# Kernel optimization log

Hardware: AMD Instinct MI355X
Metric: run time of the kernel (lower is better)

## Reference

```python
import jax, jax.numpy as jnp
import numpy as np

B, S, E, H = 2, 2048, 1024, 16
D = E // H  # head_dim = 64


def setup_inputs() -> dict:
    key = jax.random.key(0)
    ks = jax.random.split(key, 6)
    scale = 1.0 / np.sqrt(E)
    return {
        "x": jax.random.normal(ks[0], (B, S, E), dtype=jnp.float32),
        "Wqkv_w": jax.random.normal(ks[1], (3 * E, E), dtype=jnp.float32) * scale,
        "Wqkv_b": jax.random.normal(ks[2], (3 * E,), dtype=jnp.float32) * 0.01,
        "out_w": jax.random.normal(ks[3], (E, E), dtype=jnp.float32) * scale,
        "out_b": jax.random.normal(ks[4], (E,), dtype=jnp.float32) * 0.01,
        "distance_decay": jax.random.normal(ks[5], (1,), dtype=jnp.float32),
    }


def reference(x, Wqkv_w, Wqkv_b, out_w, out_b, distance_decay):
    b, s, e = x.shape
    # fused QKV projection: (b, s, 3e) -> three (b, h, s, d)
    qkv = x @ Wqkv_w.T + Wqkv_b
    qkv = qkv.reshape(b, s, 3, H, D).transpose(2, 0, 3, 1, 4)  # (3, b, h, s, d)
    q, k, v = qkv[0], qkv[1], qkv[2]
    # scores scaled by 1/sqrt(head_dim)
    scores = jnp.einsum("bhsd,bhtd->bhst", q, k) / jnp.sqrt(jnp.asarray(D, x.dtype))
    # multiplicative exponential distance decay: exp(-|a| * |i-j|)
    idx = jnp.arange(s, dtype=x.dtype)
    dist = jnp.abs(idx[:, None] - idx[None, :])  # (s, s)
    decay = jnp.exp(-jnp.abs(distance_decay[0]) * dist)
    scores = scores * decay  # broadcast over (b, h)
    attn = jax.nn.softmax(scores, axis=-1)
    out = jnp.einsum("bhst,bhtd->bhsd", attn, v)  # (b, h, s, d)
    out = out.transpose(0, 2, 1, 3).reshape(b, s, e)  # (b, s, e)
    return out @ out_w.T + out_b
```

## Files before the change

### kernel.cpp

```cpp
#include <hip/hip_runtime.h>
#include <hip/hip_bf16.h>

#define BN 2
#define SDIM 2048
#define EDIM 1024
#define HN 16
#define DDIM 64

typedef __attribute__((ext_vector_type(8))) short bfrag;
typedef __attribute__((ext_vector_type(4))) float ffrag;

__device__ __forceinline__ ffrag mfma16(bfrag a, bfrag b, ffrag c) {
    return __builtin_amdgcn_mfma_f32_16x16x32_bf16(a, b, c, 0, 0, 0);
}

__device__ __forceinline__ ushort f2bf(float f) {
    union { float f; unsigned u; } un;
    un.f = f;
    unsigned u = un.u;
    u += 0x7fffu + ((u >> 16) & 1u);
    return (ushort)(u >> 16);
}

__device__ __forceinline__ uint pkbf2(float a, float b) {
    __hip_bfloat162 h = __float22bfloat162_rn(make_float2(a, b));
    union { __hip_bfloat162 h; uint u; } cv;
    cv.h = h;
    return cv.u;
}

__device__ __forceinline__ void gld16(const void* g, void* l) {
    __builtin_amdgcn_global_load_lds((const __attribute__((address_space(1))) void*)g,
                                     (__attribute__((address_space(3))) void*)l,
                                     16, 0, 0);
}

__global__ __launch_bounds__(256) void to_bf16_3(const float* __restrict__ a, ushort* __restrict__ oa, int na,
                                                 const float* __restrict__ b, ushort* __restrict__ ob, int nb,
                                                 const float* __restrict__ c, ushort* __restrict__ oc, int nc) {
    int i = (blockIdx.x * 256 + threadIdx.x) * 4;
    const float* src;
    ushort* dst;
    if (i < na)                { src = a + i;            dst = oa + i; }
    else if (i < na + nb)      { src = b + (i - na);     dst = ob + (i - na); }
    else if (i < na + nb + nc) { src = c + (i - na - nb); dst = oc + (i - na - nb); }
    else return;
    float4 v = *(const float4*)src;
    uint2 u;
    u.x = pkbf2(v.x, v.y);
    u.y = pkbf2(v.z, v.w);
    *(uint2*)dst = u;
}

template <int MODE, int MI>
__global__ __launch_bounds__(256) void gemm_bt(const ushort* __restrict__ A,
                                               const ushort* __restrict__ Bt,
                                               const float* __restrict__ bias,
                                               void* __restrict__ Cout,
                                               int M, int N, int K) {
    __shared__ ushort As[MI * 32 * 32];
    __shared__ ushort Bs[128 * 32];

    const int tid  = threadIdx.x;
    const int wave = tid >> 6;
    const int lane = tid & 63;
    const int ln16 = lane & 15;
    const int quad = lane >> 4;
    const int wm = wave >> 1, wn = wave & 1;
    const int bm = blockIdx.x * (MI * 32);
    const int bn = blockIdx.y * 128;

    ffrag acc[MI][4];
#pragma unroll
    for (int mi = 0; mi < MI; ++mi)
#pragma unroll
        for (int ni = 0; ni < 4; ++ni)
            acc[mi][ni] = (ffrag){0.f, 0.f, 0.f, 0.f};

    for (int k0 = 0; k0 < K; k0 += 32) {
#pragma unroll
        for (int p = 0; p < MI / 2; ++p) {
            int g0 = p * 256 + wave * 64;
            int g  = g0 + lane;
            int r  = g >> 2;
            int c  = ((g & 3) - (r >> 1)) & 3;
            gld16(A + (size_t)(bm + r) * K + k0 + c * 8, (ushort*)As + g0 * 8);
        }
#pragma unroll
        for (int p = 0; p < 2; ++p) {
            int g0 = p * 256 + wave * 64;
            int g  = g0 + lane;
            int r  = g >> 2;
            int c  = ((g & 3) - (r >> 1)) & 3;
            gld16(Bt + (size_t)(bn + r) * K + k0 + c * 8, (ushort*)Bs + g0 * 8);
        }
        __syncthreads();

        bfrag af[MI], bf[4];
#pragma unroll
        for (int mi = 0; mi < MI; ++mi) {
            int r = wm * (MI * 16) + mi * 16 + ln16;
            af[mi] = *(const bfrag*)&As[r * 32 + ((quad + (r >> 1)) & 3) * 8];
        }
#pragma unroll
        for (int ni = 0; ni < 4; ++ni) {
            int r = wn * 64 + ni * 16 + ln16;
            bf[ni] = *(const bfrag*)&Bs[r * 32 + ((quad + (r >> 1)) & 3) * 8];
        }
#pragma unroll
        for (int mi = 0; mi < MI; ++mi)
#pragma unroll
            for (int ni = 0; ni < 4; ++ni)
                acc[mi][ni] = mfma16(af[mi], bf[ni], acc[mi][ni]);
        __syncthreads();
    }

#pragma unroll
    for (int mi = 0; mi < MI; ++mi) {
#pragma unroll
        for (int ni = 0; ni < 4; ++ni) {
            int col = bn + wn * 64 + ni * 16 + ln16;
            float bc = bias[col];
            int row0 = bm + wm * (MI * 16) + mi * 16 + quad * 4;
            if (MODE == 0) {
#pragma unroll
                for (int reg = 0; reg < 4; ++reg)
                    ((float*)Cout)[(size_t)(row0 + reg) * N + col] = acc[mi][ni][reg] + bc;
            } else {
                int which = col >> 10;
                int rem = col & 1023;
                int h = rem >> 6;
                int d = rem & 63;
                int b = row0 >> 11;
                int s0 = row0 & 2047;
                if (which == 2) {
                    float v0 = acc[mi][ni][0] + bc, v1 = acc[mi][ni][1] + bc;
                    float v2 = acc[mi][ni][2] + bc, v3 = acc[mi][ni][3] + bc;
                    uint2 pk;
                    pk.x = pkbf2(v0, v1);
                    pk.y = pkbf2(v2, v3);
                    size_t dst = 2ull * (BN * HN * SDIM * DDIM) +
                                 (((size_t)(b * HN + h)) * DDIM + d) * SDIM + s0;
                    *(uint2*)((ushort*)Cout + dst) = pk;
                } else {
                    float sc = (which == 0) ? 0.125f : 1.f;
#pragma unroll
                    for (int reg = 0; reg < 4; ++reg) {
                        float v = (acc[mi][ni][reg] + bc) * sc;
                        size_t dst = (size_t)which * (BN * HN * SDIM * DDIM) +
                                     (((size_t)(b * HN + h)) * SDIM + s0 + reg) * DDIM + d;
                        ((ushort*)Cout)[dst] = f2bf(v);
                    }
                }
            }
        }
    }
}

__global__ __launch_bounds__(64) void vsum_prefix(const ushort* __restrict__ Vtb,
                                                  float* __restrict__ PS) {
    const int bh = blockIdx.x;
    const int d  = threadIdx.x;
    const ushort* row = Vtb + ((size_t)bh * DDIM + d) * SDIM;
    float* ps = PS + (size_t)bh * 33 * 64;
    float run = 0.f;
    for (int k = 0; k < 32; ++k) {
        ps[k * 64 + d] = run;
        float s = 0.f;
#pragma unroll
        for (int j = 0; j < 64; j += 8) {
            uint4 v = *(const uint4*)(row + k * 64 + j);
            ushort tmp[8];
            *(uint4*)tmp = v;
#pragma unroll
            for (int e = 0; e < 8; ++e) {
                union { float f; uint u; } c;
                c.u = ((uint)tmp[e]) << 16;
                s += c.f;
            }
        }
        run += s;
    }
    ps[32 * 64 + d] = run;
}

__global__ __launch_bounds__(512, 4) void flash_attn(const ushort* __restrict__ Qb,
                                                     const ushort* __restrict__ Kb,
                                                     const ushort* __restrict__ Vtb,
                                                     const float* __restrict__ decay_ptr,
                                                     const float* __restrict__ PS,
                                                     ushort* __restrict__ Ob) {
    __shared__ ushort KVs[2][2][4096];
    __shared__ ushort Pb[128][72];
    __shared__ float  Fv[64];

    const int tid  = threadIdx.x;
    const int wave = tid >> 6;
    const int lane = tid & 63;
    const int ln16 = lane & 15;
    const int quad = lane >> 4;

    const int bh = blockIdx.y;
    const int q0 = blockIdx.x * 128;
    const size_t head_off = (size_t)bh * SDIM * DDIM;
    const float absa = fabsf(decay_ptr[0]);
    const float LOG2E = 1.442695041f;
    const float M0L2 = -17.3123404f;
    const float E12 = 6.144212353e-6f;

    int Dstar = (absa > 1e-5f) ? (int)ceilf(16.0f / absa) : (4 * SDIM);
    int lo = q0 - 63 - Dstar; if (lo < 0) lo = 0;
    int hi = q0 + 127 + Dstar; if (hi > SDIM - 1) hi = SDIM - 1;
    const int tlo = lo >> 6;
    const int thi = hi >> 6;
    const int ntiles = thi - tlo + 1;

    if (tid < 64) {
        const float* ps = PS + (size_t)bh * 33 * 64;
        Fv[tid] = ps[tlo * 64 + tid] + ps[32 * 64 + tid] - ps[(thi + 1) * 64 + tid];
    }

    auto stageKV = [&](int t0, int buf) {
        int g0 = wave * 64;
        int g  = g0 + lane;
        int r  = g >> 3;
        int c  = (g - r) & 7;
        gld16(Kb  + head_off + (size_t)(t0 + r) * DDIM + c * 8,
              (ushort*)&KVs[buf][0][0] + g0 * 8);
        gld16(Vtb + head_off + (size_t)r * SDIM + t0 + c * 8,
              (ushort*)&KVs[buf][1][0] + g0 * 8);
    };

#pragma unroll
    for (int p = 0; p < 2; ++p) {
        int idx = p * 512 + tid;
        int r = idx >> 3, c = (idx & 7) * 8;
        *(uint4*)&Pb[r][c] = *(const uint4*)(Qb + head_off + (size_t)(q0 + r) * DDIM + c);
    }
    stageKV(tlo * 64, 0);
    __syncthreads();

    bfrag aq[2];
#pragma unroll
    for (int kb = 0; kb < 2; ++kb)
        aq[kb] = *(const bfrag*)&Pb[wave * 16 + ln16][kb * 32 + quad * 8];

    bfrag ones;
#pragma unroll
    for (int i = 0; i < 8; ++i) ones[i] = (short)0x3F80;

    float EcB[4], FcB[4], Epw[4], Fpw[4];
#pragma unroll
    for (int reg = 0; reg < 4; ++reg) {
        int cr = quad * 4 + reg;
        EcB[reg] = __expf(-absa * (float)(15 - cr));
        FcB[reg] = __expf(-absa * (float)cr);
    }
#pragma unroll
    for (int ni = 0; ni < 4; ++ni) {
        Epw[ni] = __expf(-absa * (float)(16 * (3 - ni)));
        Fpw[ni] = __expf(-absa * (float)(16 * ni));
    }
    const float Er = __expf(-absa * (float)ln16);
    const float Fr = __expf(-absa * (float)(15 - ln16));

    ffrag lacc = (ffrag){0.f, 0.f, 0.f, 0.f};
    ffrag o[4];
#pragma unroll
    for (int ni = 0; ni < 4; ++ni) o[ni] = (ffrag){0.f, 0.f, 0.f, 0.f};

    const int m = wave * 16 + ln16;

    for (int it = 0; it < ntiles; ++it) {
        const int t0 = (tlo + it) * 64;
        const int buf = it & 1;
        if (it + 1 < ntiles) stageKV(t0 + 64, buf ^ 1);

        const ushort* Kt = &KVs[buf][0][0];
        const ushort* Vt = &KVs[buf][1][0];

        ffrag sc[4];
#pragma unroll
        for (int ni = 0; ni < 4; ++ni) {
            ffrag a = (ffrag){0.f, 0.f, 0.f, 0.f};
            const int rk = ni * 16 + ln16;
#pragma unroll
            for (int kb = 0; kb < 2; ++kb) {
                bfrag kf = *(const bfrag*)&Kt[rk * 64 + ((kb * 4 + quad + rk) & 7) * 8];
                a = mfma16(kf, aq[kb], a);
            }
            sc[ni] = a;
        }

        const int ds = q0 + wave * 16 - t0;
        float hh = 0.f;
        if (ds >= 64)       hh = __expf(-absa * (float)(ds - 63)) * Er * LOG2E;
        else if (ds <= -16) hh = __expf(-absa * (float)(-ds - 15)) * Fr * LOG2E;

#pragma unroll
        for (int ni = 0; ni < 4; ++ni) {
            float f0, f1, f2, f3;
            if (ds >= 64) {
                float hn = hh * Epw[ni];
                f0 = hn * EcB[0]; f1 = hn * EcB[1]; f2 = hn * EcB[2]; f3 = hn * EcB[3];
            } else if (ds <= -16) {
                float hn = hh * Fpw[ni];
                f0 = hn * FcB[0]; f1 = hn * FcB[1]; f2 = hn * FcB[2]; f3 = hn * FcB[3];
            } else {
                int c0 = ni * 16 + quad * 4;
                f0 = __expf(-absa * fabsf((float)(ds + ln16 - c0)))     * LOG2E;
                f1 = __expf(-absa * fabsf((float)(ds + ln16 - c0 - 1))) * LOG2E;
                f2 = __expf(-absa * fabsf((float)(ds + ln16 - c0 - 2))) * LOG2E;
                f3 = __expf(-absa * fabsf((float)(ds + ln16 - c0 - 3))) * LOG2E;
            }
            float p0 = exp2f(fmaf(sc[ni][0], f0, M0L2));
            float p1 = exp2f(fmaf(sc[ni][1], f1, M0L2));
            float p2 = exp2f(fmaf(sc[ni][2], f2, M0L2));
            float p3 = exp2f(fmaf(sc[ni][3], f3, M0L2));
            uint2 pk;
            pk.x = pkbf2(p0, p1);
            pk.y = pkbf2(p2, p3);
            *(uint2*)&Pb[m][ni * 16 + quad * 4] = pk;
        }

        bfrag ap[2];
#pragma unroll
        for (int kb = 0; kb < 2; ++kb)
            ap[kb] = *(const bfrag*)&Pb[m][kb * 32 + quad * 8];

#pragma unroll
        for (int kb = 0; kb < 2; ++kb)
            lacc = mfma16(ones, ap[kb], lacc);
#pragma unroll
        for (int ni = 0; ni < 4; ++ni) {
            const int rv = ni * 16 + ln16;
#pragma unroll
            for (int kb = 0; kb < 2; ++kb) {
                bfrag vf = *(const bfrag*)&Vt[rv * 64 + ((kb * 4 + quad + rv) & 7) * 8];
                o[ni] = mfma16(vf, ap[kb], o[ni]);
            }
        }
        __syncthreads();
    }

    const float farl = E12 * (float)(SDIM - 64 * ntiles);
    const float inv = 1.f / (lacc[0] + farl);
    const int b = bh / HN, h = bh % HN;
    const int s = q0 + m;
    ushort* dst = Ob + ((size_t)(b * SDIM + s)) * EDIM + h * DDIM + quad * 4;
#pragma unroll
    for (int ni = 0; ni < 4; ++ni) {
        int d0 = ni * 16 + quad * 4;
        float v0 = (o[ni][0] + E12 * Fv[d0 + 0]) * inv;
        float v1 = (o[ni][1] + E12 * Fv[d0 + 1]) * inv;
        float v2 = (o[ni][2] + E12 * Fv[d0 + 2]) * inv;
        float v3 = (o[ni][3] + E12 * Fv[d0 + 3]) * inv;
        uint2 pk;
        pk.x = pkbf2(v0, v1);
        pk.y = pkbf2(v2, v3);
        *(uint2*)(dst + ni * 16) = pk;
    }
}

extern "C" void kernel_launch(void* const* d_in, const int* in_sizes, int n_in,
                              void* d_out, int out_size, void* d_ws, size_t ws_size,
                              hipStream_t stream) {
    const float* x      = (const float*)d_in[0];
    const float* Wqkv_w = (const float*)d_in[1];
    const float* Wqkv_b = (const float*)d_in[2];
    const float* out_w  = (const float*)d_in[3];
    const float* out_b  = (const float*)d_in[4];
    const float* dd     = (const float*)d_in[5];

    char* ws = (char*)d_ws;
    const size_t MB = 1024 * 1024;
    ushort* xb    = (ushort*)(ws + 0 * MB);
    ushort* wqkvb = (ushort*)(ws + 8 * MB);
    ushort* owb   = (ushort*)(ws + 14 * MB);
    ushort* qkvb  = (ushort*)(ws + 16 * MB);
    ushort* ob    = (ushort*)(ws + 40 * MB);
    float*  PSp   = (float*)(ws + 0 * MB);

    const int n_x = BN * SDIM * EDIM;
    const int n_w = 3 * EDIM * EDIM;
    const int n_o = EDIM * EDIM;
    const int HSD = BN * HN * SDIM * DDIM;

    to_bf16_3<<<(n_x + n_w + n_o) / 1024, 256, 0, stream>>>(
        x, xb, n_x, Wqkv_w, wqkvb, n_w, out_w, owb, n_o);

    gemm_bt<1, 4><<<dim3(32, 24), 256, 0, stream>>>(xb, wqkvb, Wqkv_b, (void*)qkvb,
                                                    BN * SDIM, 3 * EDIM, EDIM);

    vsum_prefix<<<32, 64, 0, stream>>>(qkvb + 2 * HSD, PSp);

    flash_attn<<<dim3(SDIM / 128, BN * HN), 512, 0, stream>>>(
        qkvb, qkvb + HSD, qkvb + 2 * HSD, dd, PSp, ob);

    gemm_bt<0, 2><<<dim3(64, 8), 256, 0, stream>>>(ob, owb, out_b, d_out,
                                                   BN * SDIM, EDIM, EDIM);
}
```

Baseline: 196.6 us.

## Double GEMM K-tile to 64 and parallelize V tile sums

The GEMM kernels now stage a 64-wide K slice per iteration, with a new XOR-style swizzle, and run two MFMA sub-steps between barriers. This halves the number of __syncthreads and global-load rounds per output tile, at the cost of doubling LDS use per block, which may lower occupancy. The serial per-head prefix-sum kernel (32 blocks of 64 threads) is replaced by a parallel per-tile sum kernel over a 32x8 grid. The attention kernel now adds up the out-of-band tile sums itself with short loops, instead of reading prefix differences.

Result: faster. 163.8 us (-16.7%).

```diff
diff --git a/kernel.cpp b/kernel.cpp
--- a/kernel.cpp
+++ b/kernel.cpp
@@ -58,8 +58,8 @@
                                                const float* __restrict__ bias,
                                                void* __restrict__ Cout,
                                                int M, int N, int K) {
-    __shared__ ushort As[MI * 32 * 32];
-    __shared__ ushort Bs[128 * 32];
+    __shared__ ushort As[MI * 32 * 64];
+    __shared__ ushort Bs[128 * 64];
 
     const int tid  = threadIdx.x;
     const int wave = tid >> 6;
@@ -77,41 +77,44 @@
         for (int ni = 0; ni < 4; ++ni)
             acc[mi][ni] = (ffrag){0.f, 0.f, 0.f, 0.f};
 
-    for (int k0 = 0; k0 < K; k0 += 32) {
-#pragma unroll
-        for (int p = 0; p < MI / 2; ++p) {
+    for (int k0 = 0; k0 < K; k0 += 64) {
+#pragma unroll
+        for (int p = 0; p < MI; ++p) {
             int g0 = p * 256 + wave * 64;
             int g  = g0 + lane;
-            int r  = g >> 2;
-            int c  = ((g & 3) - (r >> 1)) & 3;
+            int r  = g >> 3;
+            int c  = ((g & 7) - r) & 7;
             gld16(A + (size_t)(bm + r) * K + k0 + c * 8, (ushort*)As + g0 * 8);
         }
 #pragma unroll
-        for (int p = 0; p < 2; ++p) {
+        for (int p = 0; p < 4; ++p) {
             int g0 = p * 256 + wave * 64;
             int g  = g0 + lane;
-            int r  = g >> 2;
-            int c  = ((g & 3) - (r >> 1)) & 3;
+            int r  = g >> 3;
+            int c  = ((g & 7) - r) & 7;
             gld16(Bt + (size_t)(bn + r) * K + k0 + c * 8, (ushort*)Bs + g0 * 8);
         }
         __syncthreads();
 
-        bfrag af[MI], bf[4];
-#pragma unroll
-        for (int mi = 0; mi < MI; ++mi) {
-            int r = wm * (MI * 16) + mi * 16 + ln16;
-            af[mi] = *(const bfrag*)&As[r * 32 + ((quad + (r >> 1)) & 3) * 8];
-        }
-#pragma unroll
-        for (int ni = 0; ni < 4; ++ni) {
-            int r = wn * 64 + ni * 16 + ln16;
-            bf[ni] = *(const bfrag*)&Bs[r * 32 + ((quad + (r >> 1)) & 3) * 8];
-        }
-#pragma unroll
-        for (int mi = 0; mi < MI; ++mi)
-#pragma unroll
-            for (int ni = 0; ni < 4; ++ni)
-                acc[mi][ni] = mfma16(af[mi], bf[ni], acc[mi][ni]);
+#pragma unroll
+        for (int kb = 0; kb < 2; ++kb) {
+            bfrag af[MI], bf[4];
+#pragma unroll
+            for (int mi = 0; mi < MI; ++mi) {
+                int r = wm * (MI * 16) + mi * 16 + ln16;
+                af[mi] = *(const bfrag*)&As[r * 64 + ((kb * 4 + quad + r) & 7) * 8];
+            }
+#pragma unroll
+            for (int ni = 0; ni < 4; ++ni) {
+                int r = wn * 64 + ni * 16 + ln16;
+                bf[ni] = *(const bfrag*)&Bs[r * 64 + ((kb * 4 + quad + r) & 7) * 8];
+            }
+#pragma unroll
+            for (int mi = 0; mi < MI; ++mi)
+#pragma unroll
+                for (int ni = 0; ni < 4; ++ni)
+                    acc[mi][ni] = mfma16(af[mi], bf[ni], acc[mi][ni]);
+        }
         __syncthreads();
     }
 
@@ -157,38 +160,33 @@
     }
 }
 
-__global__ __launch_bounds__(64) void vsum_prefix(const ushort* __restrict__ Vtb,
-                                                  float* __restrict__ PS) {
-    const int bh = blockIdx.x;
-    const int d  = threadIdx.x;
-    const ushort* row = Vtb + ((size_t)bh * DDIM + d) * SDIM;
-    float* ps = PS + (size_t)bh * 33 * 64;
-    float run = 0.f;
-    for (int k = 0; k < 32; ++k) {
-        ps[k * 64 + d] = run;
-        float s = 0.f;
-#pragma unroll
-        for (int j = 0; j < 64; j += 8) {
-            uint4 v = *(const uint4*)(row + k * 64 + j);
-            ushort tmp[8];
-            *(uint4*)tmp = v;
-#pragma unroll
-            for (int e = 0; e < 8; ++e) {
-                union { float f; uint u; } c;
-                c.u = ((uint)tmp[e]) << 16;
-                s += c.f;
-            }
-        }
-        run += s;
-    }
-    ps[32 * 64 + d] = run;
+__global__ __launch_bounds__(256) void vsum_tiles(const ushort* __restrict__ Vtb,
+                                                  float* __restrict__ T) {
+    const int bh   = blockIdx.x;
+    const int tile = blockIdx.y * 4 + (threadIdx.x >> 6);
+    const int d    = threadIdx.x & 63;
+    const ushort* row = Vtb + ((size_t)bh * DDIM + d) * SDIM + tile * 64;
+    float s = 0.f;
+#pragma unroll
+    for (int j = 0; j < 64; j += 8) {
+        uint4 v = *(const uint4*)(row + j);
+        ushort tmp[8];
+        *(uint4*)tmp = v;
+#pragma unroll
+        for (int e = 0; e < 8; ++e) {
+            union { float f; uint u; } c;
+            c.u = ((uint)tmp[e]) << 16;
+            s += c.f;
+        }
+    }
+    T[((size_t)bh * 32 + tile) * 64 + d] = s;
 }
 
 __global__ __launch_bounds__(512, 4) void flash_attn(const ushort* __restrict__ Qb,
                                                      const ushort* __restrict__ Kb,
                                                      const ushort* __restrict__ Vtb,
                                                      const float* __restrict__ decay_ptr,
-                                                     const float* __restrict__ PS,
+                                                     const float* __restrict__ T,
                                                      ushort* __restrict__ Ob) {
     __shared__ ushort KVs[2][2][4096];
     __shared__ ushort Pb[128][72];
@@ -216,8 +214,11 @@
     const int ntiles = thi - tlo + 1;
 
     if (tid < 64) {
-        const float* ps = PS + (size_t)bh * 33 * 64;
-        Fv[tid] = ps[tlo * 64 + tid] + ps[32 * 64 + tid] - ps[(thi + 1) * 64 + tid];
+        const float* Tp = T + (size_t)bh * 32 * 64;
+        float s = 0.f;
+        for (int k = 0; k < tlo; ++k)      s += Tp[k * 64 + tid];
+        for (int k = thi + 1; k < 32; ++k) s += Tp[k * 64 + tid];
+        Fv[tid] = s;
     }
 
     auto stageKV = [&](int t0, int buf) {
@@ -379,7 +380,7 @@
     ushort* owb   = (ushort*)(ws + 14 * MB);
     ushort* qkvb  = (ushort*)(ws + 16 * MB);
     ushort* ob    = (ushort*)(ws + 40 * MB);
-    float*  PSp   = (float*)(ws + 0 * MB);
+    float*  Tp    = (float*)(ws + 0 * MB);
 
     const int n_x = BN * SDIM * EDIM;
     const int n_w = 3 * EDIM * EDIM;
@@ -392,10 +393,10 @@
     gemm_bt<1, 4><<<dim3(32, 24), 256, 0, stream>>>(xb, wqkvb, Wqkv_b, (void*)qkvb,
                                                     BN * SDIM, 3 * EDIM, EDIM);
 
-    vsum_prefix<<<32, 64, 0, stream>>>(qkvb + 2 * HSD, PSp);
+    vsum_tiles<<<dim3(32, 8), 256, 0, stream>>>(qkvb + 2 * HSD, Tp);
 
     flash_attn<<<dim3(SDIM / 128, BN * HN), 512, 0, stream>>>(
-        qkvb, qkvb + HSD, qkvb + 2 * HSD, dd, PSp, ob);
+        qkvb, qkvb + HSD, qkvb + 2 * HSD, dd, Tp, ob);
 
     gemm_bt<0, 2><<<dim3(64, 8), 256, 0, stream>>>(ob, owb, out_b, d_out,
                                                    BN * SDIM, EDIM, EDIM);
```
